# Kernel optimization log

Measured on AMD Instinct MI355X. Metric: run time of the kernel, lower is better.

The kernel has to match this reference:

```python
import jax, jax.numpy as jnp
import numpy as np

EPS_F = 1e-6  # epsilon used when normalizing F^T F (as in EIGNN/MGNNI)


def _g(F):
    # g(F) = F^T F / (||F^T F||_F + eps): symmetric PSD, spectral radius <= 1
    FF = F.T @ F
    return FF / (jnp.linalg.norm(FF) + EPS_F)


def setup_inputs() -> dict:
    m, n = 128, 8192
    key = jax.random.key(0)
    k1, k2, k3, k4 = jax.random.split(key, 4)
    X = jax.random.normal(k1, (m, n), dtype=jnp.float32)
    # learned mixing matrix, init 1/sqrt(m) * randn as in __init__
    F = (1.0 / np.sqrt(m)) * jax.random.normal(k2, (m, m), dtype=jnp.float32)
    # precomputed eigendecomposition of the (normalized) adjacency S:
    # eigenvector matrix Q_S (n,n) and eigenvalues Lambda_S stored as (n,1)
    Q_S = jax.random.normal(k3, (n, n), dtype=jnp.float32) / np.sqrt(n)
    Lambda_S = (0.99 * (2.0 * jax.random.uniform(k4, (n, 1), dtype=jnp.float32) - 1.0))
    gamma = jnp.float32(0.8)
    return {"X": X, "F": F, "Q_S": Q_S, "Lambda_S": Lambda_S, "gamma": gamma}


def reference(X, F, Q_S, Lambda_S, gamma):
    # IDMFunction.forward: closed-form solve of Z = gamma * g(F) Z S + X
    # via eigendecompositions g(F) = Q_F diag(Lam_F) Q_F^T, S = Q_S diag(Lam_S) Q_S^T
    Lam_F, Q_F = jnp.linalg.eigh(_g(F))                         # (m,), (m,m)
    # G[i,j] = 1 / (1 - gamma * Lam_F[i] * Lam_S[j])            # (m,n)
    G = 1.0 / (1.0 - gamma * Lam_F[:, None] * Lambda_S.reshape(1, -1))
    # Z = Q_F (G * (Q_F^T X Q_S)) Q_S^T                          # (m,n)
    Z = Q_F @ (G * (Q_F.T @ X @ Q_S)) @ Q_S.T
    return Z
```

## Files before the change

### kernel.cpp

```cpp
#include <hip/hip_runtime.h>
#include <math.h>

#define EPS_F 1e-6f

typedef __attribute__((ext_vector_type(8))) short short8;
typedef __attribute__((ext_vector_type(4))) float f32x4;
typedef unsigned long long ull;

static __device__ __forceinline__ unsigned short f2bf(float f) {
    unsigned u = __float_as_uint(f);
    u += 0x7fff + ((u >> 16) & 1);
    return (unsigned short)(u >> 16);
}
static __device__ __forceinline__ ull pack4(float a, float b, float c, float d) {
    return (ull)f2bf(a) | ((ull)f2bf(b) << 16) | ((ull)f2bf(c) << 32) | ((ull)f2bf(d) << 48);
}
static __device__ __forceinline__ float bf2f(unsigned short s) {
    return __uint_as_float(((unsigned)s) << 16);
}


__global__ void kff(const float* __restrict__ F, float* __restrict__ FF) {
    int i = blockIdx.x, j = threadIdx.x;
    float s = 0.f;
    for (int k = 0; k < 128; ++k) s += F[k*128 + i] * F[k*128 + j];
    FF[i*128 + j] = s;
}

__global__ void knorm(const float* __restrict__ FF, float* __restrict__ inv) {
    float s = 0.f;
    for (int idx = threadIdx.x; idx < 128*128; idx += 256) { float v = FF[idx]; s += v*v; }
    for (int o = 32; o > 0; o >>= 1) s += __shfl_down(s, o);
    __shared__ float wsum[4];
    int lane = threadIdx.x & 63, w = threadIdx.x >> 6;
    if (lane == 0) wsum[w] = s;
    __syncthreads();
    if (threadIdx.x == 0) inv[0] = 1.f / (sqrtf(wsum[0]+wsum[1]+wsum[2]+wsum[3]) + EPS_F);
}

__global__ void kxbf(const float* __restrict__ X, short* __restrict__ Xb) {
    int i = blockIdx.x*blockDim.x + threadIdx.x;
    const float4* p = (const float4*)(X + (size_t)i*8);
    float4 v0 = p[0], v1 = p[1];
    *(ull*)&Xb[(size_t)i*8    ] = pack4(v0.x, v0.y, v0.z, v0.w);
    *(ull*)&Xb[(size_t)i*8 + 4] = pack4(v1.x, v1.y, v1.z, v1.w);
}

template<bool TRANSB>
__global__ __launch_bounds__(256) void gemm_s(
    const short* __restrict__ Ab, const float* __restrict__ Qg,
    float* __restrict__ Cp, int N, int K)
{
    constexpr int LDT = 48;
    __shared__ short As[2][128 * LDT];
    __shared__ short Bs[2][64 * LDT];

    const int t    = threadIdx.x;
    const int lane = t & 63;
    const int w    = t >> 6;
    const int wm   = (w >> 1) * 64;
    const int wn   = (w & 1)  * 32;
    const int l16  = lane & 15;
    const int lq   = lane >> 4;
    const int n0   = blockIdx.x * 64;
    const int KC   = K >> 3;
    const int kb   = blockIdx.y * KC;

    float* Cout = Cp + (size_t)blockIdx.y * (128 * 8192);

    const int ar0 = t >> 2, ako = (t & 3) * 8;
    const int br0 = t >> 3, bko = (t & 7) * 4;
    const int bn  = t & 63, bkh = t >> 6;

    f32x4 acc[4][2];
    #pragma unroll
    for (int i = 0; i < 4; ++i) { acc[i][0] = (f32x4){0,0,0,0}; acc[i][1] = (f32x4){0,0,0,0}; }

    short8 sa0, sa1;
    float4 sb0, sb1;
    float  sbt[8];

    const int NS = KC / 32;

    {
        const int k0 = kb;
        sa0 = *(const short8*)&Ab[(size_t)ar0*K + k0 + ako];
        sa1 = *(const short8*)&Ab[(size_t)(ar0+64)*K + k0 + ako];
        if (TRANSB) {
            sb0 = *(const float4*)&Qg[(size_t)(n0+br0   )*K + k0 + bko];
            sb1 = *(const float4*)&Qg[(size_t)(n0+br0+32)*K + k0 + bko];
        } else {
            #pragma unroll
            for (int j = 0; j < 8; ++j)
                sbt[j] = Qg[(size_t)(k0 + bkh*8 + j)*N + n0 + bn];
        }
        *(short8*)&As[0][ar0*LDT + ako]      = sa0;
        *(short8*)&As[0][(ar0+64)*LDT + ako] = sa1;
        if (TRANSB) {
            *(ull*)&Bs[0][br0*LDT + bko]      = pack4(sb0.x, sb0.y, sb0.z, sb0.w);
            *(ull*)&Bs[0][(br0+32)*LDT + bko] = pack4(sb1.x, sb1.y, sb1.z, sb1.w);
        } else {
            short8 p;
            #pragma unroll
            for (int j = 0; j < 8; ++j) p[j] = (short)f2bf(sbt[j]);
            *(short8*)&Bs[0][bn*LDT + bkh*8] = p;
        }
    }
    __syncthreads();

    for (int ks = 0; ks < NS; ++ks) {
        const int cur = ks & 1;
        const bool more = (ks + 1 < NS);

        if (more) {
            const int k0 = kb + (ks + 1) * 32;
            sa0 = *(const short8*)&Ab[(size_t)ar0*K + k0 + ako];
            sa1 = *(const short8*)&Ab[(size_t)(ar0+64)*K + k0 + ako];
            if (TRANSB) {
                sb0 = *(const float4*)&Qg[(size_t)(n0+br0   )*K + k0 + bko];
                sb1 = *(const float4*)&Qg[(size_t)(n0+br0+32)*K + k0 + bko];
            } else {
                #pragma unroll
                for (int j = 0; j < 8; ++j)
                    sbt[j] = Qg[(size_t)(k0 + bkh*8 + j)*N + n0 + bn];
            }
        }

        short8 af[4], bfr[2];
        #pragma unroll
        for (int mt = 0; mt < 4; ++mt)
            af[mt] = *(const short8*)&As[cur][(wm + mt*16 + l16)*LDT + lq*8];
        bfr[0] = *(const short8*)&Bs[cur][(wn      + l16)*LDT + lq*8];
        bfr[1] = *(const short8*)&Bs[cur][(wn + 16 + l16)*LDT + lq*8];
        #pragma unroll
        for (int mt = 0; mt < 4; ++mt) {
            acc[mt][0] = __builtin_amdgcn_mfma_f32_16x16x32_bf16(af[mt], bfr[0], acc[mt][0], 0, 0, 0);
            acc[mt][1] = __builtin_amdgcn_mfma_f32_16x16x32_bf16(af[mt], bfr[1], acc[mt][1], 0, 0, 0);
        }

        if (more) {
            const int nxt = cur ^ 1;
            *(short8*)&As[nxt][ar0*LDT + ako]      = sa0;
            *(short8*)&As[nxt][(ar0+64)*LDT + ako] = sa1;
            if (TRANSB) {
                *(ull*)&Bs[nxt][br0*LDT + bko]      = pack4(sb0.x, sb0.y, sb0.z, sb0.w);
                *(ull*)&Bs[nxt][(br0+32)*LDT + bko] = pack4(sb1.x, sb1.y, sb1.z, sb1.w);
            } else {
                short8 p;
                #pragma unroll
                for (int j = 0; j < 8; ++j) p[j] = (short)f2bf(sbt[j]);
                *(short8*)&Bs[nxt][bn*LDT + bkh*8] = p;
            }
            __syncthreads();
        }
    }

    #pragma unroll
    for (int mt = 0; mt < 4; ++mt)
        #pragma unroll
        for (int nt = 0; nt < 2; ++nt)
            #pragma unroll
            for (int r = 0; r < 4; ++r)
                Cout[(size_t)(wm + mt*16 + lq*4 + r)*N + n0 + wn + nt*16 + l16] = acc[mt][nt][r];
}

__global__ __launch_bounds__(512) void horner_fused(
    const float* __restrict__ FF, const float* __restrict__ invn,
    const float* __restrict__ lam, const float* __restrict__ gam,
    const float* __restrict__ Yp, short* __restrict__ Rg, int N)
{
    constexpr int LDT = 136;
    constexpr int T = 14;
    constexpr int SPL = 8;
    __shared__ short Abf[128 * LDT];
    __shared__ short Rs[32 * LDT];

    const int t    = threadIdx.x;
    const int lane = t & 63;
    const int w    = t >> 6;
    const int wm   = (w >> 1) * 32;
    const int wn   = (w & 1) * 16;
    const int l16  = lane & 15;
    const int lq   = lane >> 4;
    const int j0   = blockIdx.x * 32;

    #pragma unroll
    for (int i = 0; i < 8; ++i) {
        int flat = t + i*512;
        int m = flat >> 5, k4 = flat & 31;
        float4 v = *(const float4*)&FF[m*128 + k4*4];
        *(ull*)&Abf[m*LDT + k4*4] = pack4(v.x, v.y, v.z, v.w);
    }
    {
        int j = t & 31, mg = t >> 5;
        float vv[8];
        #pragma unroll
        for (int r2 = 0; r2 < 8; ++r2) {
            size_t idx = (size_t)(mg*8 + r2)*N + j0 + j;
            float s = 0.f;
            #pragma unroll
            for (int sp = 0; sp < SPL; ++sp) s += Yp[(size_t)sp*(128*8192) + idx];
            vv[r2] = s;
        }
        *(ull*)&Rs[j*LDT + mg*8    ] = pack4(vv[0], vv[1], vv[2], vv[3]);
        *(ull*)&Rs[j*LDT + mg*8 + 4] = pack4(vv[4], vv[5], vv[6], vv[7]);
    }
    __syncthreads();

    const int col = j0 + wn + l16;
    float yreg[2][4];
    #pragma unroll
    for (int mt = 0; mt < 2; ++mt)
        #pragma unroll
        for (int r = 0; r < 4; ++r)
            yreg[mt][r] = bf2f((unsigned short)Rs[(wn + l16)*LDT + wm + mt*16 + lq*4 + r]);
    const float s = gam[0] * lam[col] * invn[0];

    for (int it = 0; it < T; ++it) {
        f32x4 racc[2];
        racc[0] = (f32x4){0,0,0,0};
        racc[1] = (f32x4){0,0,0,0};
        #pragma unroll
        for (int kq = 0; kq < 4; ++kq) {
            short8 b  = *(const short8*)&Rs[(wn + l16)*LDT + kq*32 + lq*8];
            short8 a0 = *(const short8*)&Abf[(wm      + l16)*LDT + kq*32 + lq*8];
            short8 a1 = *(const short8*)&Abf[(wm + 16 + l16)*LDT + kq*32 + lq*8];
            racc[0] = __builtin_amdgcn_mfma_f32_16x16x32_bf16(a0, b, racc[0], 0, 0, 0);
            racc[1] = __builtin_amdgcn_mfma_f32_16x16x32_bf16(a1, b, racc[1], 0, 0, 0);
        }
        __syncthreads();
        #pragma unroll
        for (int mt = 0; mt < 2; ++mt) {
            float r0 = yreg[mt][0] + s*racc[mt][0];
            float r1 = yreg[mt][1] + s*racc[mt][1];
            float r2 = yreg[mt][2] + s*racc[mt][2];
            float r3 = yreg[mt][3] + s*racc[mt][3];
            if (it < T-1) {
                *(ull*)&Rs[(wn + l16)*LDT + wm + mt*16 + lq*4] = pack4(r0, r1, r2, r3);
            } else {
                int row = wm + mt*16 + lq*4;
                Rg[(size_t)(row+0)*N + col] = (short)f2bf(r0);
                Rg[(size_t)(row+1)*N + col] = (short)f2bf(r1);
                Rg[(size_t)(row+2)*N + col] = (short)f2bf(r2);
                Rg[(size_t)(row+3)*N + col] = (short)f2bf(r3);
            }
        }
        if (it < T-1) __syncthreads();
    }
}

__global__ __launch_bounds__(256) void zred(const float* __restrict__ Zp,
                                            float* __restrict__ Z) {
    int i = (blockIdx.x*blockDim.x + threadIdx.x) * 4;
    f32x4 s = (f32x4){0,0,0,0};
    #pragma unroll
    for (int sp = 0; sp < 8; ++sp) {
        const float4 v = *(const float4*)&Zp[(size_t)sp*(128*8192) + i];
        s[0] += v.x; s[1] += v.y; s[2] += v.z; s[3] += v.w;
    }
    *(f32x4*)&Z[i] = s;
}


extern "C" void kernel_launch(void* const* d_in, const int* in_sizes, int n_in,
                              void* d_out, int out_size, void* d_ws, size_t ws_size,
                              hipStream_t stream) {
    const float* X   = (const float*)d_in[0];
    const float* F   = (const float*)d_in[1];
    const float* Q   = (const float*)d_in[2];
    const float* lam = (const float*)d_in[3];
    const float* gam = (const float*)d_in[4];
    float* Z = (float*)d_out;

    const int N = 8192, K = 8192;

    char* ws = (char*)d_ws;
    float* FF  = (float*)(ws);
    float* inv = (float*)(ws + 65536);
    short* Xb  = (short*)(ws + 131072);
    short* Rg  = (short*)(ws + 131072 + 2097152);
    float* Yp  = (float*)(ws + 131072 + 4194304);
    float* Zp  = (float*)(ws + 131072 + 4194304 + 33554432);

    hipLaunchKernelGGL(kff,   dim3(128), dim3(128), 0, stream, F, FF);
    hipLaunchKernelGGL(knorm, dim3(1),   dim3(256), 0, stream, FF, inv);
    hipLaunchKernelGGL(kxbf,  dim3(512), dim3(256), 0, stream, X, Xb);

    hipLaunchKernelGGL((gemm_s<false>), dim3(128, 8), dim3(256), 0, stream,
                       Xb, Q, Yp, N, K);

    hipLaunchKernelGGL(horner_fused, dim3(256), dim3(512), 0, stream,
                       FF, inv, lam, gam, Yp, Rg, N);

    hipLaunchKernelGGL((gemm_s<true>), dim3(128, 8), dim3(256), 0, stream,
                       Rg, Q, Zp, N, K);

    hipLaunchKernelGGL(zred, dim3(1024), dim3(256), 0, stream, Zp, Z);
}
```

Measured before the change: 186.0 us.

## Specialize the two Q GEMMs with separate tilings, split-K and swizzled shared memory

```diff
diff --git a/kernel.cpp b/kernel.cpp
--- a/kernel.cpp
+++ b/kernel.cpp
@@ -46,112 +46,191 @@
     *(ull*)&Xb[(size_t)i*8 + 4] = pack4(v1.x, v1.y, v1.z, v1.w);
 }
 
-template<bool TRANSB>
-__global__ __launch_bounds__(256) void gemm_s(
-    const short* __restrict__ Ab, const float* __restrict__ Qg,
-    float* __restrict__ Cp, int N, int K)
+__global__ __launch_bounds__(512) void gemm1(
+    const short* __restrict__ Xb, const float* __restrict__ Q,
+    float* __restrict__ Yp, int N, int K)
 {
-    constexpr int LDT = 48;
+    constexpr int LDT = 40;
     __shared__ short As[2][128 * LDT];
-    __shared__ short Bs[2][64 * LDT];
+    __shared__ short Bs[2][128 * LDT];
+
+    const int t    = threadIdx.x;
+    const int lane = t & 63;
+    const int w    = t >> 6;
+    const int wm   = (w >> 2) * 64;
+    const int wn   = (w & 3) * 32;
+    const int l16  = lane & 15;
+    const int lq   = lane >> 4;
+    const int n0   = blockIdx.x * 128;
+    const int KC   = 512;
+    const int kb   = blockIdx.y * KC;
+    constexpr int NS = 16;
+
+    float* Cout = Yp + (size_t)blockIdx.y * (128 * 8192);
+
+    const int bn  = t & 127, bkq = t >> 7;
+    const int am  = t >> 2,  ako = (t & 3) * 8;
+
+    f32x4 acc[4][2];
+    #pragma unroll
+    for (int i = 0; i < 4; ++i) { acc[i][0] = (f32x4){0,0,0,0}; acc[i][1] = (f32x4){0,0,0,0}; }
+
+    float bv[8];
+    short8 sa;
+
+    {
+        const int k0 = kb;
+        #pragma unroll
+        for (int j = 0; j < 8; ++j)
+            bv[j] = Q[(size_t)(k0 + bkq*8 + j)*N + n0 + bn];
+        sa = *(const short8*)&Xb[(size_t)am*K + k0 + ako];
+        short8 p;
+        #pragma unroll
+        for (int j = 0; j < 8; ++j) p[j] = (short)f2bf(bv[j]);
+        *(short8*)&Bs[0][bn*LDT + bkq*8] = p;
+        *(short8*)&As[0][am*LDT + ako]   = sa;
+    }
+    __syncthreads();
+
+    for (int ks = 0; ks < NS; ++ks) {
+        const int cur = ks & 1;
+        const bool more = (ks + 1 < NS);
+
+        if (more) {
+            const int k0 = kb + (ks + 1) * 32;
+            #pragma unroll
+            for (int j = 0; j < 8; ++j)
+                bv[j] = Q[(size_t)(k0 + bkq*8 + j)*N + n0 + bn];
+            sa = *(const short8*)&Xb[(size_t)am*K + k0 + ako];
+        }
+
+        short8 af[4], bf[2];
+        #pragma unroll
+        for (int mt = 0; mt < 4; ++mt)
+            af[mt] = *(const short8*)&As[cur][(wm + mt*16 + l16)*LDT + lq*8];
+        bf[0] = *(const short8*)&Bs[cur][(wn      + l16)*LDT + lq*8];
+        bf[1] = *(const short8*)&Bs[cur][(wn + 16 + l16)*LDT + lq*8];
+        #pragma unroll
+        for (int mt = 0; mt < 4; ++mt) {
+            acc[mt][0] = __builtin_amdgcn_mfma_f32_16x16x32_bf16(af[mt], bf[0], acc[mt][0], 0, 0, 0);
+            acc[mt][1] = __builtin_amdgcn_mfma_f32_16x16x32_bf16(af[mt], bf[1], acc[mt][1], 0, 0, 0);
+        }
+
+        if (more) {
+            const int nxt = cur ^ 1;
+            short8 p;
+            #pragma unroll
+            for (int j = 0; j < 8; ++j) p[j] = (short)f2bf(bv[j]);
+            *(short8*)&Bs[nxt][bn*LDT + bkq*8] = p;
+            *(short8*)&As[nxt][am*LDT + ako]   = sa;
+            __syncthreads();
+        }
+    }
+
+    #pragma unroll
+    for (int mt = 0; mt < 4; ++mt)
+        #pragma unroll
+        for (int nt = 0; nt < 2; ++nt)
+            #pragma unroll
+            for (int r = 0; r < 4; ++r)
+                Cout[(size_t)(wm + mt*16 + lq*4 + r)*N + n0 + wn + nt*16 + l16] = acc[mt][nt][r];
+}
+
+__global__ __launch_bounds__(256) void gemm2(
+    const short* __restrict__ Rb, const float* __restrict__ Q,
+    float* __restrict__ Zp, int N, int K)
+{
+    constexpr int LDK = 136;
+    __shared__ short As2[128 * LDK];
+    __shared__ short Bs2[64 * LDK];
 
     const int t    = threadIdx.x;
     const int lane = t & 63;
     const int w    = t >> 6;
     const int wm   = (w >> 1) * 64;
-    const int wn   = (w & 1)  * 32;
+    const int wn   = (w & 1) * 32;
     const int l16  = lane & 15;
     const int lq   = lane >> 4;
     const int n0   = blockIdx.x * 64;
-    const int KC   = K >> 3;
+    const int KC   = 1024;
     const int kb   = blockIdx.y * KC;
-
-    float* Cout = Cp + (size_t)blockIdx.y * (128 * 8192);
-
-    const int ar0 = t >> 2, ako = (t & 3) * 8;
-    const int br0 = t >> 3, bko = (t & 7) * 4;
-    const int bn  = t & 63, bkh = t >> 6;
+    constexpr int NS = 8;
+
+    float* Cout = Zp + (size_t)blockIdx.y * (128 * 8192);
+
+    const int brow = t >> 4, bq = t & 15;
+    const int am2  = t >> 1, ko2 = (t & 1) * 64;
 
     f32x4 acc[4][2];
     #pragma unroll
     for (int i = 0; i < 4; ++i) { acc[i][0] = (f32x4){0,0,0,0}; acc[i][1] = (f32x4){0,0,0,0}; }
 
-    short8 sa0, sa1;
-    float4 sb0, sb1;
-    float  sbt[8];
-
-    const int NS = KC / 32;
+    float4 sb[8];
+    short8 sa[8];
 
     {
         const int k0 = kb;
-        sa0 = *(const short8*)&Ab[(size_t)ar0*K + k0 + ako];
-        sa1 = *(const short8*)&Ab[(size_t)(ar0+64)*K + k0 + ako];
-        if (TRANSB) {
-            sb0 = *(const float4*)&Qg[(size_t)(n0+br0   )*K + k0 + bko];
-            sb1 = *(const float4*)&Qg[(size_t)(n0+br0+32)*K + k0 + bko];
-        } else {
+        #pragma unroll
+        for (int ps = 0; ps < 4; ++ps)
+            #pragma unroll
+            for (int h = 0; h < 2; ++h)
+                sb[ps*2+h] = *(const float4*)&Q[(size_t)(n0 + ps*16 + brow)*K + k0 + bq*4 + h*64];
+        #pragma unroll
+        for (int j = 0; j < 8; ++j)
+            sa[j] = *(const short8*)&Rb[(size_t)am2*K + k0 + ko2 + j*8];
+    }
+
+    for (int ks = 0; ks < NS; ++ks) {
+        __syncthreads();
+
+        #pragma unroll
+        for (int ps = 0; ps < 4; ++ps)
+            #pragma unroll
+            for (int h = 0; h < 2; ++h) {
+                int row = ps*16 + brow;
+                int sh  = (bq*4 + h*64) ^ ((row & 3) << 4);
+                float4 v = sb[ps*2+h];
+                *(ull*)&Bs2[row*LDK + sh] = pack4(v.x, v.y, v.z, v.w);
+            }
+        #pragma unroll
+        for (int j = 0; j < 8; ++j) {
+            int sh = (ko2 + j*8) ^ ((am2 & 3) << 4);
+            *(short8*)&As2[am2*LDK + sh] = sa[j];
+        }
+        __syncthreads();
+
+        if (ks + 1 < NS) {
+            const int k0 = kb + (ks + 1) * 128;
+            #pragma unroll
+            for (int ps = 0; ps < 4; ++ps)
+                #pragma unroll
+                for (int h = 0; h < 2; ++h)
+                    sb[ps*2+h] = *(const float4*)&Q[(size_t)(n0 + ps*16 + brow)*K + k0 + bq*4 + h*64];
             #pragma unroll
             for (int j = 0; j < 8; ++j)
-                sbt[j] = Qg[(size_t)(k0 + bkh*8 + j)*N + n0 + bn];
-        }
-        *(short8*)&As[0][ar0*LDT + ako]      = sa0;
-        *(short8*)&As[0][(ar0+64)*LDT + ako] = sa1;
-        if (TRANSB) {
-            *(ull*)&Bs[0][br0*LDT + bko]      = pack4(sb0.x, sb0.y, sb0.z, sb0.w);
-            *(ull*)&Bs[0][(br0+32)*LDT + bko] = pack4(sb1.x, sb1.y, sb1.z, sb1.w);
-        } else {
-            short8 p;
-            #pragma unroll
-            for (int j = 0; j < 8; ++j) p[j] = (short)f2bf(sbt[j]);
-            *(short8*)&Bs[0][bn*LDT + bkh*8] = p;
-        }
-    }
-    __syncthreads();
-
-    for (int ks = 0; ks < NS; ++ks) {
-        const int cur = ks & 1;
-        const bool more = (ks + 1 < NS);
-
-        if (more) {
-            const int k0 = kb + (ks + 1) * 32;
-            sa0 = *(const short8*)&Ab[(size_t)ar0*K + k0 + ako];
-            sa1 = *(const short8*)&Ab[(size_t)(ar0+64)*K + k0 + ako];
-            if (TRANSB) {
-                sb0 = *(const float4*)&Qg[(size_t)(n0+br0   )*K + k0 + bko];
-                sb1 = *(const float4*)&Qg[(size_t)(n0+br0+32)*K + k0 + bko];
-            } else {
-                #pragma unroll
-                for (int j = 0; j < 8; ++j)
-                    sbt[j] = Qg[(size_t)(k0 + bkh*8 + j)*N + n0 + bn];
-            }
-        }
-
-        short8 af[4], bfr[2];
-        #pragma unroll
-        for (int mt = 0; mt < 4; ++mt)
-            af[mt] = *(const short8*)&As[cur][(wm + mt*16 + l16)*LDT + lq*8];
-        bfr[0] = *(const short8*)&Bs[cur][(wn      + l16)*LDT + lq*8];
-        bfr[1] = *(const short8*)&Bs[cur][(wn + 16 + l16)*LDT + lq*8];
-        #pragma unroll
-        for (int mt = 0; mt < 4; ++mt) {
-            acc[mt][0] = __builtin_amdgcn_mfma_f32_16x16x32_bf16(af[mt], bfr[0], acc[mt][0], 0, 0, 0);
-            acc[mt][1] = __builtin_amdgcn_mfma_f32_16x16x32_bf16(af[mt], bfr[1], acc[mt][1], 0, 0, 0);
-        }
-
-        if (more) {
-            const int nxt = cur ^ 1;
-            *(short8*)&As[nxt][ar0*LDT + ako]      = sa0;
-            *(short8*)&As[nxt][(ar0+64)*LDT + ako] = sa1;
-            if (TRANSB) {
-                *(ull*)&Bs[nxt][br0*LDT + bko]      = pack4(sb0.x, sb0.y, sb0.z, sb0.w);
-                *(ull*)&Bs[nxt][(br0+32)*LDT + bko] = pack4(sb1.x, sb1.y, sb1.z, sb1.w);
-            } else {
-                short8 p;
-                #pragma unroll
-                for (int j = 0; j < 8; ++j) p[j] = (short)f2bf(sbt[j]);
-                *(short8*)&Bs[nxt][bn*LDT + bkh*8] = p;
-            }
-            __syncthreads();
+                sa[j] = *(const short8*)&Rb[(size_t)am2*K + k0 + ko2 + j*8];
+        }
+
+        #pragma unroll
+        for (int ksub = 0; ksub < 4; ++ksub) {
+            short8 af[4], bf[2];
+            #pragma unroll
+            for (int mt = 0; mt < 4; ++mt) {
+                int row = wm + mt*16 + l16;
+                int sh  = (ksub*32 + lq*8) ^ ((row & 3) << 4);
+                af[mt] = *(const short8*)&As2[row*LDK + sh];
+            }
+            #pragma unroll
+            for (int nt = 0; nt < 2; ++nt) {
+                int row = wn + nt*16 + l16;
+                int sh  = (ksub*32 + lq*8) ^ ((row & 3) << 4);
+                bf[nt] = *(const short8*)&Bs2[row*LDK + sh];
+            }
+            #pragma unroll
+            for (int mt = 0; mt < 4; ++mt) {
+                acc[mt][0] = __builtin_amdgcn_mfma_f32_16x16x32_bf16(af[mt], bf[0], acc[mt][0], 0, 0, 0);
+                acc[mt][1] = __builtin_amdgcn_mfma_f32_16x16x32_bf16(af[mt], bf[1], acc[mt][1], 0, 0, 0);
+            }
         }
     }
 
@@ -171,7 +250,7 @@
 {
     constexpr int LDT = 136;
     constexpr int T = 14;
-    constexpr int SPL = 8;
+    constexpr int SPL = 16;
     __shared__ short Abf[128 * LDT];
     __shared__ short Rs[32 * LDT];
 
@@ -278,22 +357,20 @@
     float* FF  = (float*)(ws);
     float* inv = (float*)(ws + 65536);
     short* Xb  = (short*)(ws + 131072);
-    short* Rg  = (short*)(ws + 131072 + 2097152);
-    float* Yp  = (float*)(ws + 131072 + 4194304);
-    float* Zp  = (float*)(ws + 131072 + 4194304 + 33554432);
+    short* Rg  = (short*)(ws + 2228224);
+    float* Yp  = (float*)(ws + 4325376);
+    float* Zp  = (float*)(ws + 4325376 + 67108864);
 
     hipLaunchKernelGGL(kff,   dim3(128), dim3(128), 0, stream, F, FF);
     hipLaunchKernelGGL(knorm, dim3(1),   dim3(256), 0, stream, FF, inv);
     hipLaunchKernelGGL(kxbf,  dim3(512), dim3(256), 0, stream, X, Xb);
 
-    hipLaunchKernelGGL((gemm_s<false>), dim3(128, 8), dim3(256), 0, stream,
-                       Xb, Q, Yp, N, K);
+    hipLaunchKernelGGL(gemm1, dim3(64, 16), dim3(512), 0, stream, Xb, Q, Yp, N, K);
 
     hipLaunchKernelGGL(horner_fused, dim3(256), dim3(512), 0, stream,
                        FF, inv, lam, gam, Yp, Rg, N);
 
-    hipLaunchKernelGGL((gemm_s<true>), dim3(128, 8), dim3(256), 0, stream,
-                       Rg, Q, Zp, N, K);
+    hipLaunchKernelGGL(gemm2, dim3(128, 8), dim3(256), 0, stream, Rg, Q, Zp, N, K);
 
     hipLaunchKernelGGL(zred, dim3(1024), dim3(256), 0, stream, Zp, Z);
 }
```

Result: slower. 198.8 us (+6.9%).

## Triple-buffer split-K GEMM pipeline and double split-K for first GEMM

Applied to the files above, without the earlier changes.

```diff
diff --git a/kernel.cpp b/kernel.cpp
--- a/kernel.cpp
+++ b/kernel.cpp
@@ -47,13 +47,15 @@
 }
 
 template<bool TRANSB>
-__global__ __launch_bounds__(256) void gemm_s(
+__global__ __launch_bounds__(256) void gemm_p3(
     const short* __restrict__ Ab, const float* __restrict__ Qg,
-    float* __restrict__ Cp, int N, int K)
+    float* __restrict__ Cp, int N, int K, int KC)
 {
-    constexpr int LDT = 48;
-    __shared__ short As[2][128 * LDT];
-    __shared__ short Bs[2][64 * LDT];
+    constexpr int LDT = 40;
+    constexpr int ASZ = 128 * LDT;
+    constexpr int BSZ = 64 * LDT;
+    __shared__ short As[3 * ASZ];
+    __shared__ short Bs[3 * BSZ];
 
     const int t    = threadIdx.x;
     const int lane = t & 63;
@@ -63,8 +65,8 @@
     const int l16  = lane & 15;
     const int lq   = lane >> 4;
     const int n0   = blockIdx.x * 64;
-    const int KC   = K >> 3;
     const int kb   = blockIdx.y * KC;
+    const int NS   = KC >> 5;
 
     float* Cout = Cp + (size_t)blockIdx.y * (128 * 8192);
 
@@ -76,84 +78,78 @@
     #pragma unroll
     for (int i = 0; i < 4; ++i) { acc[i][0] = (f32x4){0,0,0,0}; acc[i][1] = (f32x4){0,0,0,0}; }
 
-    short8 sa0, sa1;
-    float4 sb0, sb1;
-    float  sbt[8];
-
-    const int NS = KC / 32;
-
-    {
-        const int k0 = kb;
-        sa0 = *(const short8*)&Ab[(size_t)ar0*K + k0 + ako];
-        sa1 = *(const short8*)&Ab[(size_t)(ar0+64)*K + k0 + ako];
-        if (TRANSB) {
-            sb0 = *(const float4*)&Qg[(size_t)(n0+br0   )*K + k0 + bko];
-            sb1 = *(const float4*)&Qg[(size_t)(n0+br0+32)*K + k0 + bko];
-        } else {
-            #pragma unroll
-            for (int j = 0; j < 8; ++j)
-                sbt[j] = Qg[(size_t)(k0 + bkh*8 + j)*N + n0 + bn];
-        }
-        *(short8*)&As[0][ar0*LDT + ako]      = sa0;
-        *(short8*)&As[0][(ar0+64)*LDT + ako] = sa1;
-        if (TRANSB) {
-            *(ull*)&Bs[0][br0*LDT + bko]      = pack4(sb0.x, sb0.y, sb0.z, sb0.w);
-            *(ull*)&Bs[0][(br0+32)*LDT + bko] = pack4(sb1.x, sb1.y, sb1.z, sb1.w);
-        } else {
-            short8 p;
-            #pragma unroll
-            for (int j = 0; j < 8; ++j) p[j] = (short)f2bf(sbt[j]);
-            *(short8*)&Bs[0][bn*LDT + bkh*8] = p;
-        }
-    }
+    short8 saA0, saA1, saB0, saB1;
+    float4 sbA0, sbA1, sbB0, sbB1;
+    float  sbtA[8], sbtB[8];
+
+#define LOAD_T(k0, SA0, SA1, SB0, SB1, SBT) do {                                  \
+        SA0 = *(const short8*)&Ab[(size_t)ar0*K + (k0) + ako];                    \
+        SA1 = *(const short8*)&Ab[(size_t)(ar0+64)*K + (k0) + ako];               \
+        if constexpr (TRANSB) {                                                   \
+            SB0 = *(const float4*)&Qg[(size_t)(n0+br0   )*K + (k0) + bko];        \
+            SB1 = *(const float4*)&Qg[(size_t)(n0+br0+32)*K + (k0) + bko];        \
+        } else {                                                                  \
+            _Pragma("unroll")                                                     \
+            for (int j = 0; j < 8; ++j)                                           \
+                SBT[j] = Qg[(size_t)((k0) + bkh*8 + j)*N + n0 + bn];              \
+        }                                                                         \
+    } while (0)
+
+#define WRITE_T(buf, SA0, SA1, SB0, SB1, SBT) do {                                \
+        short* asb = &As[(buf)*ASZ];                                              \
+        short* bsb = &Bs[(buf)*BSZ];                                              \
+        *(short8*)&asb[ar0*LDT + ako]      = SA0;                                 \
+        *(short8*)&asb[(ar0+64)*LDT + ako] = SA1;                                 \
+        if constexpr (TRANSB) {                                                   \
+            *(ull*)&bsb[br0*LDT + bko]      = pack4(SB0.x, SB0.y, SB0.z, SB0.w);  \
+            *(ull*)&bsb[(br0+32)*LDT + bko] = pack4(SB1.x, SB1.y, SB1.z, SB1.w);  \
+        } else {                                                                  \
+            short8 p;                                                             \
+            _Pragma("unroll")                                                     \
+            for (int j = 0; j < 8; ++j) p[j] = (short)f2bf(SBT[j]);               \
+            *(short8*)&bsb[bn*LDT + bkh*8] = p;                                   \
+        }                                                                         \
+    } while (0)
+
+#define MFMA_T(buf) do {                                                          \
+        const short* asb = &As[(buf)*ASZ];                                        \
+        const short* bsb = &Bs[(buf)*BSZ];                                        \
+        short8 af[4], bfr[2];                                                     \
+        _Pragma("unroll")                                                         \
+        for (int mt = 0; mt < 4; ++mt)                                            \
+            af[mt] = *(const short8*)&asb[(wm + mt*16 + l16)*LDT + lq*8];         \
+        bfr[0] = *(const short8*)&bsb[(wn      + l16)*LDT + lq*8];                \
+        bfr[1] = *(const short8*)&bsb[(wn + 16 + l16)*LDT + lq*8];                \
+        _Pragma("unroll")                                                         \
+        for (int mt = 0; mt < 4; ++mt) {                                          \
+            acc[mt][0] = __builtin_amdgcn_mfma_f32_16x16x32_bf16(af[mt], bfr[0], acc[mt][0], 0, 0, 0); \
+            acc[mt][1] = __builtin_amdgcn_mfma_f32_16x16x32_bf16(af[mt], bfr[1], acc[mt][1], 0, 0, 0); \
+        }                                                                         \
+    } while (0)
+
+    LOAD_T(kb,      saA0, saA1, sbA0, sbA1, sbtA);
+    LOAD_T(kb + 32, saB0, saB1, sbB0, sbB1, sbtB);
+    WRITE_T(0, saA0, saA1, sbA0, sbA1, sbtA);
     __syncthreads();
 
-    for (int ks = 0; ks < NS; ++ks) {
-        const int cur = ks & 1;
-        const bool more = (ks + 1 < NS);
-
-        if (more) {
-            const int k0 = kb + (ks + 1) * 32;
-            sa0 = *(const short8*)&Ab[(size_t)ar0*K + k0 + ako];
-            sa1 = *(const short8*)&Ab[(size_t)(ar0+64)*K + k0 + ako];
-            if (TRANSB) {
-                sb0 = *(const float4*)&Qg[(size_t)(n0+br0   )*K + k0 + bko];
-                sb1 = *(const float4*)&Qg[(size_t)(n0+br0+32)*K + k0 + bko];
-            } else {
-                #pragma unroll
-                for (int j = 0; j < 8; ++j)
-                    sbt[j] = Qg[(size_t)(k0 + bkh*8 + j)*N + n0 + bn];
-            }
-        }
-
-        short8 af[4], bfr[2];
-        #pragma unroll
-        for (int mt = 0; mt < 4; ++mt)
-            af[mt] = *(const short8*)&As[cur][(wm + mt*16 + l16)*LDT + lq*8];
-        bfr[0] = *(const short8*)&Bs[cur][(wn      + l16)*LDT + lq*8];
-        bfr[1] = *(const short8*)&Bs[cur][(wn + 16 + l16)*LDT + lq*8];
-        #pragma unroll
-        for (int mt = 0; mt < 4; ++mt) {
-            acc[mt][0] = __builtin_amdgcn_mfma_f32_16x16x32_bf16(af[mt], bfr[0], acc[mt][0], 0, 0, 0);
-            acc[mt][1] = __builtin_amdgcn_mfma_f32_16x16x32_bf16(af[mt], bfr[1], acc[mt][1], 0, 0, 0);
-        }
-
-        if (more) {
-            const int nxt = cur ^ 1;
-            *(short8*)&As[nxt][ar0*LDT + ako]      = sa0;
-            *(short8*)&As[nxt][(ar0+64)*LDT + ako] = sa1;
-            if (TRANSB) {
-                *(ull*)&Bs[nxt][br0*LDT + bko]      = pack4(sb0.x, sb0.y, sb0.z, sb0.w);
-                *(ull*)&Bs[nxt][(br0+32)*LDT + bko] = pack4(sb1.x, sb1.y, sb1.z, sb1.w);
-            } else {
-                short8 p;
-                #pragma unroll
-                for (int j = 0; j < 8; ++j) p[j] = (short)f2bf(sbt[j]);
-                *(short8*)&Bs[nxt][bn*LDT + bkh*8] = p;
-            }
-            __syncthreads();
-        }
-    }
+    int b0 = 0, b1 = 1, b2 = 2;
+    for (int ks = 0; ks < NS; ks += 2) {
+        if (ks + 2 < NS) LOAD_T(kb + (ks+2)*32, saA0, saA1, sbA0, sbA1, sbtA);
+        MFMA_T(b0);
+        if (ks + 1 < NS) WRITE_T(b1, saB0, saB1, sbB0, sbB1, sbtB);
+        __syncthreads();
+
+        if (ks + 3 < NS) LOAD_T(kb + (ks+3)*32, saB0, saB1, sbB0, sbB1, sbtB);
+        MFMA_T(b1);
+        if (ks + 2 < NS) WRITE_T(b2, saA0, saA1, sbA0, sbA1, sbtA);
+        __syncthreads();
+
+        int tb = b0; b0 = b2; b2 = b1; b1 = tb;
+    }
+
+#undef LOAD_T
+#undef WRITE_T
+#undef MFMA_T
 
     #pragma unroll
     for (int mt = 0; mt < 4; ++mt)
@@ -171,7 +167,7 @@
 {
     constexpr int LDT = 136;
     constexpr int T = 14;
-    constexpr int SPL = 8;
+    constexpr int SPL = 16;
     __shared__ short Abf[128 * LDT];
     __shared__ short Rs[32 * LDT];
 
@@ -278,22 +274,22 @@
     float* FF  = (float*)(ws);
     float* inv = (float*)(ws + 65536);
     short* Xb  = (short*)(ws + 131072);
-    short* Rg  = (short*)(ws + 131072 + 2097152);
-    float* Yp  = (float*)(ws + 131072 + 4194304);
-    float* Zp  = (float*)(ws + 131072 + 4194304 + 33554432);
+    short* Rg  = (short*)(ws + 2228224);
+    float* Yp  = (float*)(ws + 4325376);
+    float* Zp  = (float*)(ws + 4325376 + 67108864);
 
     hipLaunchKernelGGL(kff,   dim3(128), dim3(128), 0, stream, F, FF);
     hipLaunchKernelGGL(knorm, dim3(1),   dim3(256), 0, stream, FF, inv);
     hipLaunchKernelGGL(kxbf,  dim3(512), dim3(256), 0, stream, X, Xb);
 
-    hipLaunchKernelGGL((gemm_s<false>), dim3(128, 8), dim3(256), 0, stream,
-                       Xb, Q, Yp, N, K);
+    hipLaunchKernelGGL((gemm_p3<false>), dim3(128, 16), dim3(256), 0, stream,
+                       Xb, Q, Yp, N, K, 512);
 
     hipLaunchKernelGGL(horner_fused, dim3(256), dim3(512), 0, stream,
                        FF, inv, lam, gam, Yp, Rg, N);
 
-    hipLaunchKernelGGL((gemm_s<true>), dim3(128, 8), dim3(256), 0, stream,
-                       Rg, Q, Zp, N, K);
+    hipLaunchKernelGGL((gemm_p3<true>), dim3(128, 8), dim3(256), 0, stream,
+                       Rg, Q, Zp, N, K, 1024);
 
     hipLaunchKernelGGL(zred, dim3(1024), dim3(256), 0, stream, Zp, Z);
 }
```

Result: slower. 219.1 us (+17.8%).
